# Performance work log

Hardware: AMD Instinct MI355X
Metric: run time of the kernel (lower is better)

The kernel has to match this reference:

```python
import jax, jax.numpy as jnp
import numpy as np

OBS, N, IN, H = 15, 50000, 2, 64
GX, GY = 4, 4
NS = 4.0


def setup_inputs() -> dict:
    key = jax.random.key(0)
    ks = jax.random.split(key, 15)
    tgt = jax.random.uniform(ks[0], (OBS, 1, IN), minval=-2.0, maxval=2.0, dtype=jnp.float32)
    oth = jax.random.uniform(ks[1], (OBS, N, IN), minval=-3.0, maxval=3.0, dtype=jnp.float32)
    mask = jax.random.randint(ks[2], (OBS, N), 0, 2, dtype=jnp.int32)
    s = 1.0 / np.sqrt(H)
    u = lambda k, shp: jax.random.uniform(k, shp, minval=-s, maxval=s, dtype=jnp.float32)
    return dict(
        observed_trajectory_target=tgt,
        observed_trajectory_others=oth,
        neighbor_mask=mask,
        W_ih=u(ks[3], (4 * H, IN)), b_ih=u(ks[4], (4 * H,)),
        W_hh=u(ks[5], (4 * H, H)), b_hh=u(ks[6], (4 * H,)),
        W1=u(ks[7], (H, H * GX * GY)), b1=u(ks[8], (H,)),
        W2=u(ks[9], (H, H)), b2=u(ks[10], (H,)),
        Wc=u(ks[11], (2, H)), bc=u(ks[12], (2,)),
    )


def reference(observed_trajectory_target, observed_trajectory_others, neighbor_mask,
              W_ih, b_ih, W_hh, b_hh, W1, b1, W2, b2, Wc, bc):
    cw = NS / GX   # cell width
    ch = NS / GY   # cell height
    hx, hy = GX // 2, GY // 2
    half = NS / 2.0

    def lstm_cell(x, h, c):
        # torch LSTMCell: gates ordered i, f, g, o
        gates = x @ W_ih.T + b_ih + h @ W_hh.T + b_hh
        i, f, g, o = jnp.split(gates, 4, axis=-1)
        c_new = jax.nn.sigmoid(f) * c + jax.nn.sigmoid(i) * jnp.tanh(g)
        h_new = jax.nn.sigmoid(o) * jnp.tanh(c_new)
        return h_new, c_new

    def step(carry, xs):
        h_t, c_t, h_o, c_o, _ = carry
        xt, xo, m = xs                      # xt: [2], xo: [N,2], m: [N]
        ref_pos = xt[:2]
        h_t, c_t = lstm_cell(xt[None, :], h_t, c_t)
        h_o, c_o = lstm_cell(xo, h_o, c_o)
        # social grid binning (dropout is identity in eval mode)
        rel = xo[:, :2] - ref_pos           # [N,2]
        within = (jnp.abs(rel[:, 0]) <= half) & (jnp.abs(rel[:, 1]) <= half)
        cx = jnp.trunc(rel[:, 0] / cw).astype(jnp.int32) + hx  # trunc == torch .long()
        cy = jnp.trunc(rel[:, 1] / ch).astype(jnp.int32) + hy
        valid = within & (cx >= 0) & (cx < GX) & (cy >= 0) & (cy < GY) & (m != 0)
        idx = jnp.where(valid, cy * GX + cx, 0)
        contrib = jnp.where(valid[:, None], h_o, 0.0)
        social = jax.ops.segment_sum(contrib, idx, num_segments=GX * GY)  # [16,H]
        sv = social.reshape(1, -1)          # [1, 16*H]
        ctx = jax.nn.relu(sv @ W1.T + b1) @ W2.T + b2
        combined = h_t + ctx
        return (h_t, c_t, h_o, c_o, combined), None

    Nn = observed_trajectory_others.shape[1]
    init = (jnp.zeros((1, H), jnp.float32), jnp.zeros((1, H), jnp.float32),
            jnp.zeros((Nn, H), jnp.float32), jnp.zeros((Nn, H), jnp.float32),
            jnp.zeros((1, H), jnp.float32))
    xs = (observed_trajectory_target[:, 0, :], observed_trajectory_others, neighbor_mask)
    (h_t, c_t, h_o, c_o, combined), _ = jax.lax.scan(step, init, xs)
    return combined @ Wc.T + bc  # [1, 2]
```

## Files before the change

kernel.cpp:

```cpp
#include <hip/hip_runtime.h>
#include <stdint.h>

#define OBS 15
#define NTOT 50000
#define HDIM 64
#define NPB 16
#define NBLK_N 3125
#define ZOFF (OBS * NPB * 8)

typedef __attribute__((ext_vector_type(8))) short short8;
typedef __attribute__((ext_vector_type(4))) float f32x4;
typedef __attribute__((ext_vector_type(4))) unsigned int u32x4;

#define KLOG2E 1.4426950408889634f
#define KLOG2E2 2.8853900817779268f

static __device__ __forceinline__ unsigned short f2bf(float f) {
  unsigned u = __float_as_uint(f);
  u += 0x7fff + ((u >> 16) & 1);
  return (unsigned short)(u >> 16);
}
static __device__ __forceinline__ float bf2f(unsigned short b) {
  return __uint_as_float(((unsigned)b) << 16);
}

#if __has_builtin(__builtin_amdgcn_exp2f)
#define EXP2F(x) __builtin_amdgcn_exp2f(x)
#else
#define EXP2F(x) exp2f(x)
#endif
#if __has_builtin(__builtin_amdgcn_rcpf)
#define RCPF(x) __builtin_amdgcn_rcpf(x)
#else
#define RCPF(x) (1.0f / (x))
#endif

static __device__ __forceinline__ float sigm(float x) {
  return RCPF(1.0f + EXP2F(-KLOG2E * x));
}
static __device__ __forceinline__ float tanh_(float x) {
  return 2.0f * RCPF(1.0f + EXP2F(-KLOG2E2 * x)) - 1.0f;
}

static __device__ __forceinline__ int hidx(int r, int cb) {
  return r * 64 + ((cb ^ (r & 7)) << 3);
}

__global__ void k_zero(float* social) {
  social[threadIdx.x] = 0.0f;
}

#define MFMA_BF16 __builtin_amdgcn_mfma_f32_16x16x32_bf16

__global__ __launch_bounds__(256, 2)
void k_neigh(
    const float* __restrict__ tgt,
    const float* __restrict__ oth,
    const int* __restrict__ mask,
    const float* __restrict__ W_ih,
    const float* __restrict__ b_ih,
    const float* __restrict__ W_hh,
    const float* __restrict__ b_hh,
    float* __restrict__ social,
    float* __restrict__ ht_out)
{
  __shared__ __align__(16) unsigned short h2[2][NPB][HDIM];
  __shared__ __align__(16) unsigned short xbf[ZOFF + 8];
  __shared__ float xs14[NPB][2];
  __shared__ float tht[HDIM];
  __shared__ float tgb[256];

  const int tid = threadIdx.x;

  if (blockIdx.x == 0) {
    const float bias = b_ih[tid] + b_hh[tid];
    const float wi0 = W_ih[tid * 2], wi1 = W_ih[tid * 2 + 1];
    const float4* Wr = (const float4*)&W_hh[tid * 64];
    if (tid < HDIM) tht[tid] = 0.0f;
    float ct = 0.0f;
    __syncthreads();
    for (int t = 0; t < OBS; ++t) {
      const float x0 = tgt[t * 2], x1 = tgt[t * 2 + 1];
      float acc = bias + x0 * wi0 + x1 * wi1;
#pragma unroll 4
      for (int k4 = 0; k4 < 16; ++k4) {
        const float4 wv = Wr[k4];
        const float4 hv = *(const float4*)&tht[k4 * 4];
        acc += wv.x * hv.x + wv.y * hv.y + wv.z * hv.z + wv.w * hv.w;
      }
      tgb[tid] = acc;
      __syncthreads();
      if (tid < HDIM) {
        const float cn =
            sigm(tgb[64 + tid]) * ct + sigm(tgb[tid]) * tanh_(tgb[128 + tid]);
        ct = cn;
        tht[tid] = sigm(tgb[192 + tid]) * tanh_(cn);
      }
      __syncthreads();
    }
    if (tid < HDIM) ht_out[tid] = tht[tid];
    return;
  }

  const int l = tid & 63;
  const int w = tid >> 6;
  const int t15 = l & 15;
  const int g4 = l >> 4;
  const int n0 = (blockIdx.x - 1) * NPB;

  if (tid < OBS * NPB) {
    const int t = tid >> 4, n = tid & 15;
    const int gn = n0 + n;
    const float x0 = oth[(t * NTOT + gn) * 2 + 0];
    const float x1 = oth[(t * NTOT + gn) * 2 + 1];
    const unsigned short xh0 = f2bf(x0);
    const unsigned short xl0 = f2bf(x0 - bf2f(xh0));
    const unsigned short xh1 = f2bf(x1);
    const unsigned short xl1 = f2bf(x1 - bf2f(xh1));
    u32x4 d;
    d.x = (unsigned)xh0 | ((unsigned)xh0 << 16);
    d.y = (unsigned)xl0 | ((unsigned)xh1 << 16);
    d.z = (unsigned)xh1 | ((unsigned)xl1 << 16);
    d.w = 0x3F803F80u;
    *(u32x4*)&xbf[tid * 8] = d;
    if (t == OBS - 1) { xs14[n][0] = x0; xs14[n][1] = x1; }
  }
  if (tid == 255) {
    u32x4 zz = {0u, 0u, 0u, 0u};
    *(u32x4*)&xbf[ZOFF] = zz;
  }
  for (int i = tid; i < NPB * HDIM / 2; i += 256) ((unsigned int*)h2[0])[i] = 0u;

  short8 Bhi0, Bhi1, Bhi2, Bhi3, Bhi4, Bhi5, Bhi6, Bhi7;
  short8 Blo0, Blo1, Blo2, Blo3, Blo4, Blo5, Blo6, Blo7;
#define LOADB(q, kt, BH, BL, SC)                                              \
  {                                                                           \
    const float* wp = &W_hh[(q * 64 + w * 16 + t15) * 64 + kt * 32 + g4 * 8]; \
    _Pragma("unroll") for (int j = 0; j < 8; ++j) {                           \
      float wv = wp[j] * (SC);                                                \
      unsigned short hi = f2bf(wv);                                           \
      unsigned short lo = f2bf(wv - bf2f(hi));                                \
      BH[j] = (short)hi;                                                      \
      BL[j] = (short)lo;                                                      \
    }                                                                         \
  }
  LOADB(0, 0, Bhi0, Blo0, -KLOG2E)  LOADB(0, 1, Bhi1, Blo1, -KLOG2E)
  LOADB(1, 0, Bhi2, Blo2, -KLOG2E)  LOADB(1, 1, Bhi3, Blo3, -KLOG2E)
  LOADB(2, 0, Bhi4, Blo4, -KLOG2E2) LOADB(2, 1, Bhi5, Blo5, -KLOG2E2)
  LOADB(3, 0, Bhi6, Blo6, -KLOG2E)  LOADB(3, 1, Bhi7, Blo7, -KLOG2E)
#undef LOADB

  short8 BX0, BX1, BX2, BX3;
  {
    u32x4 z4 = {0u, 0u, 0u, 0u};
    BX0 = BX1 = BX2 = BX3 = __builtin_bit_cast(short8, z4);
    if (g4 == 0) {
#pragma unroll
      for (int q = 0; q < 4; ++q) {
        const float sc = (q == 2) ? -KLOG2E2 : -KLOG2E;
        const int G = q * 64 + w * 16 + t15;
        const float w0 = W_ih[G * 2 + 0] * sc, w1 = W_ih[G * 2 + 1] * sc;
        const float bs = (b_ih[G] + b_hh[G]) * sc;
        const unsigned short w0h = f2bf(w0), w0l = f2bf(w0 - bf2f(w0h));
        const unsigned short w1h = f2bf(w1), w1l = f2bf(w1 - bf2f(w1h));
        const unsigned short bh = f2bf(bs), bl = f2bf(bs - bf2f(bh));
        u32x4 d;
        d.x = (unsigned)w0h | ((unsigned)w0l << 16);
        d.y = (unsigned)w0h | ((unsigned)w1h << 16);
        d.z = (unsigned)w1l | ((unsigned)w1h << 16);
        d.w = (unsigned)bh | ((unsigned)bl << 16);
        const short8 v = __builtin_bit_cast(short8, d);
        if (q == 0) BX0 = v;
        else if (q == 1) BX1 = v;
        else if (q == 2) BX2 = v;
        else BX3 = v;
      }
    }
  }

  int xo = (g4 == 0) ? (t15 * 8) : ZOFF;
  const int xst = (g4 == 0) ? (NPB * 8) : 0;

  f32x4 c = (f32x4){0.f, 0.f, 0.f, 0.f};
  const float refx = tgt[14 * 2 + 0];
  const float refy = tgt[14 * 2 + 1];

  __syncthreads();

  for (int t = 0; t < OBS; ++t) {
    const int cur = t & 1, nxt = cur ^ 1;
    const short8 Ax = *(const short8*)&xbf[xo];
    short8 A0 = *(const short8*)&h2[cur][0][hidx(t15, g4)];
    short8 A1 = *(const short8*)&h2[cur][0][hidx(t15, 4 + g4)];
    xo += xst;

    const f32x4 z = (f32x4){0.f, 0.f, 0.f, 0.f};
    f32x4 acc0 = MFMA_BF16(Ax, BX0, z, 0, 0, 0);
    f32x4 acc1 = MFMA_BF16(Ax, BX1, z, 0, 0, 0);
    f32x4 acc2 = MFMA_BF16(Ax, BX2, z, 0, 0, 0);
    f32x4 acc3 = MFMA_BF16(Ax, BX3, z, 0, 0, 0);
    acc0 = MFMA_BF16(A0, Bhi0, acc0, 0, 0, 0);
    acc1 = MFMA_BF16(A0, Bhi2, acc1, 0, 0, 0);
    acc2 = MFMA_BF16(A0, Bhi4, acc2, 0, 0, 0);
    acc3 = MFMA_BF16(A0, Bhi6, acc3, 0, 0, 0);
    acc0 = MFMA_BF16(A1, Bhi1, acc0, 0, 0, 0);
    acc1 = MFMA_BF16(A1, Bhi3, acc1, 0, 0, 0);
    acc2 = MFMA_BF16(A1, Bhi5, acc2, 0, 0, 0);
    acc3 = MFMA_BF16(A1, Bhi7, acc3, 0, 0, 0);
    acc0 = MFMA_BF16(A0, Blo0, acc0, 0, 0, 0);
    acc1 = MFMA_BF16(A0, Blo2, acc1, 0, 0, 0);
    acc2 = MFMA_BF16(A0, Blo4, acc2, 0, 0, 0);
    acc3 = MFMA_BF16(A0, Blo6, acc3, 0, 0, 0);
    acc0 = MFMA_BF16(A1, Blo1, acc0, 0, 0, 0);
    acc1 = MFMA_BF16(A1, Blo3, acc1, 0, 0, 0);
    acc2 = MFMA_BF16(A1, Blo5, acc2, 0, 0, 0);
    acc3 = MFMA_BF16(A1, Blo7, acc3, 0, 0, 0);

    if (t < OBS - 1) {
#pragma unroll
      for (int r = 0; r < 4; ++r) {
        const float ei = EXP2F(acc0[r]);
        const float ef = EXP2F(acc1[r]);
        const float eg = EXP2F(acc2[r]);
        const float eo = EXP2F(acc3[r]);
        const float sf = RCPF(1.0f + ef);
        const float rig = RCPF((1.0f + ei) * (1.0f + eg));
        const float cn = c[r] * sf + (1.0f - eg) * rig;
        c[r] = cn;
        const float ecn = EXP2F(-KLOG2E2 * cn);
        const float ro = RCPF((1.0f + eo) * (1.0f + ecn));
        const float h = (1.0f - ecn) * ro;
        const int n = g4 * 4 + r;
        const int col = w * 16 + t15;
        h2[nxt][0][hidx(n, col >> 3) + (col & 7)] = f2bf(h);
      }
      __syncthreads();
    } else {
#pragma unroll
      for (int r = 0; r < 4; ++r) {
        const float ei = EXP2F(acc0[r]);
        const float ef = EXP2F(acc1[r]);
        const float eg = EXP2F(acc2[r]);
        const float eo = EXP2F(acc3[r]);
        const float sf = RCPF(1.0f + ef);
        const float rig = RCPF((1.0f + ei) * (1.0f + eg));
        const float cn = c[r] * sf + (1.0f - eg) * rig;
        const float ecn = EXP2F(-KLOG2E2 * cn);
        const float ro = RCPF((1.0f + eo) * (1.0f + ecn));
        const float h = (1.0f - ecn) * ro;
        const int nl = g4 * 4 + r;
        const int gn = n0 + nl;
        const float rx = xs14[nl][0] - refx;
        const float ry = xs14[nl][1] - refy;
        bool ok = (fabsf(rx) <= 2.0f) && (fabsf(ry) <= 2.0f);
        const int cx = (int)truncf(rx) + 2;
        const int cy = (int)truncf(ry) + 2;
        ok = ok && (cx >= 0) && (cx < 4) && (cy >= 0) && (cy < 4);
        if (ok && mask[(OBS - 1) * NTOT + gn] != 0)
          atomicAdd(&social[(cy * 4 + cx) * HDIM + w * 16 + t15], h);
      }
    }
  }
}

__global__ __launch_bounds__(512) void k_final(
    const float* __restrict__ W1, const float* __restrict__ b1,
    const float* __restrict__ W2, const float* __restrict__ b2,
    const float* __restrict__ Wc, const float* __restrict__ bc,
    const float* __restrict__ social, const float* __restrict__ ht_g,
    float* __restrict__ out)
{
  __shared__ float sv[1024];
  __shared__ float hid[64];
  __shared__ float comb[64];
  __shared__ float ht[64];

  const int tid = threadIdx.x;
  for (int i = tid; i < 1024; i += 512) sv[i] = social[i];
  if (tid < 64) ht[tid] = ht_g[tid];
  __syncthreads();

  const int wv = tid >> 6, ln = tid & 63;
  for (int o = wv; o < 64; o += 8) {
    float p = 0.0f;
#pragma unroll
    for (int it = 0; it < 16; ++it) {
      const int j = it * 64 + ln;
      p += sv[j] * W1[o * 1024 + j];
    }
#pragma unroll
    for (int off = 32; off > 0; off >>= 1) p += __shfl_down(p, off);
    if (ln == 0) hid[o] = fmaxf(p + b1[o], 0.0f);
  }
  __syncthreads();
  for (int o = wv; o < 64; o += 8) {
    float p = hid[ln] * W2[o * 64 + ln];
#pragma unroll
    for (int off = 32; off > 0; off >>= 1) p += __shfl_down(p, off);
    if (ln == 0) comb[o] = ht[o] + p + b2[o];
  }
  __syncthreads();
  if (wv < 2) {
    float p = comb[ln] * Wc[wv * 64 + ln];
#pragma unroll
    for (int off = 32; off > 0; off >>= 1) p += __shfl_down(p, off);
    if (ln == 0) out[wv] = p + bc[wv];
  }
}

extern "C" void kernel_launch(void* const* d_in, const int* in_sizes, int n_in,
                              void* d_out, int out_size, void* d_ws, size_t ws_size,
                              hipStream_t stream) {
  const float* tgt = (const float*)d_in[0];
  const float* oth = (const float*)d_in[1];
  const int* mask = (const int*)d_in[2];
  const float* W_ih = (const float*)d_in[3];
  const float* b_ih = (const float*)d_in[4];
  const float* W_hh = (const float*)d_in[5];
  const float* b_hh = (const float*)d_in[6];
  const float* W1 = (const float*)d_in[7];
  const float* b1 = (const float*)d_in[8];
  const float* W2 = (const float*)d_in[9];
  const float* b2 = (const float*)d_in[10];
  const float* Wc = (const float*)d_in[11];
  const float* bc = (const float*)d_in[12];
  float* social = (float*)d_ws;
  float* ht = social + 1024;
  float* out = (float*)d_out;

  hipLaunchKernelGGL(k_zero, dim3(1), dim3(1024), 0, stream, social);
  hipLaunchKernelGGL(k_neigh, dim3(NBLK_N + 1), dim3(256), 0, stream,
                     tgt, oth, mask, W_ih, b_ih, W_hh, b_hh, social, ht);
  hipLaunchKernelGGL(k_final, dim3(1), dim3(512), 0, stream,
                     W1, b1, W2, b2, Wc, bc, social, ht, out);
}
```

Before: 121.6 us.

## Precompute split-bf16 recurrent weights in a prep kernel and rescale cell state

Adds a prep kernel that converts W_hh into scaled hi/lo bf16 tables once, zeroing the social buffer in the same launch. Each of the 3126 neighbor blocks then loads packed short8 vectors instead of converting 128 floats per thread itself. The LSTM cell update is also reformulated to keep the cell state pre-scaled by the exp2 constant and to merge the reciprocals into one, cutting transcendental work per element. The table path depends on the workspace being large enough and otherwise falls back to the old path; the algebraic change slightly alters rounding.

```diff
diff --git a/kernel.cpp b/kernel.cpp
--- a/kernel.cpp
+++ b/kernel.cpp
@@ -46,12 +46,27 @@
   return r * 64 + ((cb ^ (r & 7)) << 3);
 }
 
+__global__ __launch_bounds__(256) void k_prep(
+    const float* __restrict__ W_hh, float* __restrict__ social,
+    unsigned short* __restrict__ whi, unsigned short* __restrict__ wlo) {
+  const int gid = blockIdx.x * 256 + threadIdx.x;
+  if (gid < 1024) social[gid] = 0.0f;
+  const int g = gid >> 6;
+  const float sc = ((g >> 6) == 2) ? -KLOG2E2 : -KLOG2E;
+  const float wv = W_hh[gid] * sc;
+  const unsigned short hi = f2bf(wv);
+  const unsigned short lo = f2bf(wv - bf2f(hi));
+  whi[gid] = hi;
+  wlo[gid] = lo;
+}
+
 __global__ void k_zero(float* social) {
   social[threadIdx.x] = 0.0f;
 }
 
 #define MFMA_BF16 __builtin_amdgcn_mfma_f32_16x16x32_bf16
 
+template <bool TAB>
 __global__ __launch_bounds__(256, 2)
 void k_neigh(
     const float* __restrict__ tgt,
@@ -61,6 +76,8 @@
     const float* __restrict__ b_ih,
     const float* __restrict__ W_hh,
     const float* __restrict__ b_hh,
+    const unsigned short* __restrict__ whi,
+    const unsigned short* __restrict__ wlo,
     float* __restrict__ social,
     float* __restrict__ ht_out)
 {
@@ -133,22 +150,36 @@
 
   short8 Bhi0, Bhi1, Bhi2, Bhi3, Bhi4, Bhi5, Bhi6, Bhi7;
   short8 Blo0, Blo1, Blo2, Blo3, Blo4, Blo5, Blo6, Blo7;
+  if constexpr (TAB) {
+#define LOADT(q, kt, BH, BL)                                      \
+    {                                                             \
+      const int base = (q * 64 + w * 16 + t15) * 64 + kt * 32 + g4 * 8; \
+      BH = *(const short8*)&whi[base];                            \
+      BL = *(const short8*)&wlo[base];                            \
+    }
+    LOADT(0, 0, Bhi0, Blo0) LOADT(0, 1, Bhi1, Blo1)
+    LOADT(1, 0, Bhi2, Blo2) LOADT(1, 1, Bhi3, Blo3)
+    LOADT(2, 0, Bhi4, Blo4) LOADT(2, 1, Bhi5, Blo5)
+    LOADT(3, 0, Bhi6, Blo6) LOADT(3, 1, Bhi7, Blo7)
+#undef LOADT
+  } else {
 #define LOADB(q, kt, BH, BL, SC)                                              \
-  {                                                                           \
-    const float* wp = &W_hh[(q * 64 + w * 16 + t15) * 64 + kt * 32 + g4 * 8]; \
-    _Pragma("unroll") for (int j = 0; j < 8; ++j) {                           \
-      float wv = wp[j] * (SC);                                                \
-      unsigned short hi = f2bf(wv);                                           \
-      unsigned short lo = f2bf(wv - bf2f(hi));                                \
-      BH[j] = (short)hi;                                                      \
-      BL[j] = (short)lo;                                                      \
-    }                                                                         \
-  }
-  LOADB(0, 0, Bhi0, Blo0, -KLOG2E)  LOADB(0, 1, Bhi1, Blo1, -KLOG2E)
-  LOADB(1, 0, Bhi2, Blo2, -KLOG2E)  LOADB(1, 1, Bhi3, Blo3, -KLOG2E)
-  LOADB(2, 0, Bhi4, Blo4, -KLOG2E2) LOADB(2, 1, Bhi5, Blo5, -KLOG2E2)
-  LOADB(3, 0, Bhi6, Blo6, -KLOG2E)  LOADB(3, 1, Bhi7, Blo7, -KLOG2E)
+    {                                                                         \
+      const float* wp = &W_hh[(q * 64 + w * 16 + t15) * 64 + kt * 32 + g4 * 8]; \
+      _Pragma("unroll") for (int j = 0; j < 8; ++j) {                         \
+        float wv = wp[j] * (SC);                                              \
+        unsigned short hi = f2bf(wv);                                         \
+        unsigned short lo = f2bf(wv - bf2f(hi));                              \
+        BH[j] = (short)hi;                                                    \
+        BL[j] = (short)lo;                                                    \
+      }                                                                       \
+    }
+    LOADB(0, 0, Bhi0, Blo0, -KLOG2E)  LOADB(0, 1, Bhi1, Blo1, -KLOG2E)
+    LOADB(1, 0, Bhi2, Blo2, -KLOG2E)  LOADB(1, 1, Bhi3, Blo3, -KLOG2E)
+    LOADB(2, 0, Bhi4, Blo4, -KLOG2E2) LOADB(2, 1, Bhi5, Blo5, -KLOG2E2)
+    LOADB(3, 0, Bhi6, Blo6, -KLOG2E)  LOADB(3, 1, Bhi7, Blo7, -KLOG2E)
 #undef LOADB
+  }
 
   short8 BX0, BX1, BX2, BX3;
   {
@@ -181,7 +212,7 @@
   int xo = (g4 == 0) ? (t15 * 8) : ZOFF;
   const int xst = (g4 == 0) ? (NPB * 8) : 0;
 
-  f32x4 c = (f32x4){0.f, 0.f, 0.f, 0.f};
+  f32x4 cs = (f32x4){0.f, 0.f, 0.f, 0.f};
   const float refx = tgt[14 * 2 + 0];
   const float refy = tgt[14 * 2 + 1];
 
@@ -223,11 +254,13 @@
         const float ef = EXP2F(acc1[r]);
         const float eg = EXP2F(acc2[r]);
         const float eo = EXP2F(acc3[r]);
-        const float sf = RCPF(1.0f + ef);
-        const float rig = RCPF((1.0f + ei) * (1.0f + eg));
-        const float cn = c[r] * sf + (1.0f - eg) * rig;
-        c[r] = cn;
-        const float ecn = EXP2F(-KLOG2E2 * cn);
+        const float A = 1.0f + ei, B = 1.0f + eg, C = 1.0f + ef;
+        const float AB = A * B;
+        const float rr = RCPF(AB * C);
+        const float u = (eg - 1.0f) * C;
+        const float csn = (cs[r] * AB + KLOG2E2 * u) * rr;
+        cs[r] = csn;
+        const float ecn = EXP2F(csn);
         const float ro = RCPF((1.0f + eo) * (1.0f + ecn));
         const float h = (1.0f - ecn) * ro;
         const int n = g4 * 4 + r;
@@ -242,10 +275,12 @@
         const float ef = EXP2F(acc1[r]);
         const float eg = EXP2F(acc2[r]);
         const float eo = EXP2F(acc3[r]);
-        const float sf = RCPF(1.0f + ef);
-        const float rig = RCPF((1.0f + ei) * (1.0f + eg));
-        const float cn = c[r] * sf + (1.0f - eg) * rig;
-        const float ecn = EXP2F(-KLOG2E2 * cn);
+        const float A = 1.0f + ei, B = 1.0f + eg, C = 1.0f + ef;
+        const float AB = A * B;
+        const float rr = RCPF(AB * C);
+        const float u = (eg - 1.0f) * C;
+        const float csn = (cs[r] * AB + KLOG2E2 * u) * rr;
+        const float ecn = EXP2F(csn);
         const float ro = RCPF((1.0f + eo) * (1.0f + ecn));
         const float h = (1.0f - ecn) * ro;
         const int nl = g4 * 4 + r;
@@ -326,11 +361,24 @@
   const float* bc = (const float*)d_in[12];
   float* social = (float*)d_ws;
   float* ht = social + 1024;
+  unsigned short* whi = (unsigned short*)((char*)d_ws + 8192);
+  unsigned short* wlo = whi + 256 * 64;
   float* out = (float*)d_out;
 
-  hipLaunchKernelGGL(k_zero, dim3(1), dim3(1024), 0, stream, social);
-  hipLaunchKernelGGL(k_neigh, dim3(NBLK_N + 1), dim3(256), 0, stream,
-                     tgt, oth, mask, W_ih, b_ih, W_hh, b_hh, social, ht);
+  const bool tab = ws_size >= (size_t)(8192 + 2 * 256 * 64 * sizeof(unsigned short));
+
+  if (tab) {
+    hipLaunchKernelGGL(k_prep, dim3(64), dim3(256), 0, stream,
+                       W_hh, social, whi, wlo);
+    hipLaunchKernelGGL((k_neigh<true>), dim3(NBLK_N + 1), dim3(256), 0, stream,
+                       tgt, oth, mask, W_ih, b_ih, W_hh, b_hh, whi, wlo,
+                       social, ht);
+  } else {
+    hipLaunchKernelGGL(k_zero, dim3(1), dim3(1024), 0, stream, social);
+    hipLaunchKernelGGL((k_neigh<false>), dim3(NBLK_N + 1), dim3(256), 0, stream,
+                       tgt, oth, mask, W_ih, b_ih, W_hh, b_hh, whi, wlo,
+                       social, ht);
+  }
   hipLaunchKernelGGL(k_final, dim3(1), dim3(512), 0, stream,
                      W1, b1, W2, b2, Wc, bc, social, ht, out);
 }
```

New measurement: 132.1 us. 1.09x slower.
